# Kernel optimization log

Measured on AMD Instinct MI355X. Metric: run time of the kernel, lower is better.

The kernel has to match this reference:

```python
import jax, jax.numpy as jnp
import numpy as np
import math

B = 1024
G = 34  # grid_dim = 17*2
C = 4
SCENT = 19


def _scent_kernel_np():
    h = w = SCENT
    mx, my = 0.5 * h, 0.5 * w
    sx, sy = h / 4.0, w / 4.0
    x = np.linspace(0.0, h, h)
    y = np.linspace(0.0, w, w)
    X, Y = np.meshgrid(x, y, indexing='ij')
    z = (1.0 / (2.0 * math.pi * sx * sy)) * np.exp(-(((X - mx) ** 2) / (2 * sx ** 2) + ((Y - my) ** 2) / (2 * sy ** 2)))
    return (z * 80.0).astype(np.float32)


def setup_inputs() -> dict:
    key = jax.random.key(0)
    k1, k2, k3, k4 = jax.random.split(key, 4)
    cell = jax.random.uniform(k1, (B, C, G, G), dtype=jnp.float32)
    food = (jax.random.uniform(k2, (B, G, G), dtype=jnp.float32) > 0.97).astype(jnp.float32)
    fc1_w = jax.random.normal(k3, (64, 12), dtype=jnp.float32) * (1.0 / np.sqrt(12))
    fc1_b = jnp.zeros((64,), dtype=jnp.float32)
    fc2_w = jax.random.normal(k4, (4, 64), dtype=jnp.float32) * (1.0 / np.sqrt(64))
    fc2_b = jnp.zeros((4,), dtype=jnp.float32)
    scent_kernel = jnp.asarray(_scent_kernel_np())
    return {"cell": cell, "food": food, "fc1_w": fc1_w, "fc1_b": fc1_b,
            "fc2_w": fc2_w, "fc2_b": fc2_b, "scent_kernel": scent_kernel, "steps": 32}


def _conv(x, w, pad, groups):
    # x: [B, Cin, H, W], w: [Cout, Cin/groups, kh, kw]; cross-correlation like torch
    return jax.lax.conv_general_dilated(
        x, w, window_strides=(1, 1), padding=[(pad, pad), (pad, pad)],
        feature_group_count=groups, dimension_numbers=('NCHW', 'OIHW', 'NCHW'))


def _maxpool3(x):
    # 3x3 max pool, stride 1, pad 1 (pad value -inf, matching torch MaxPool2d semantics)
    return jax.lax.reduce_window(x, -jnp.inf, jax.lax.max, (1, 1, 3, 3), (1, 1, 1, 1),
                                 [(0, 0), (0, 0), (1, 1), (1, 1)])


def _forward(cell, food, fc1_w, fc1_b, fc2_w, fc2_b, scent_kernel, steps):
    dx = jnp.outer(jnp.array([1., 2., 1.], jnp.float32), jnp.array([-1., 0., 1.], jnp.float32)) / 8.0
    dy = dx.T
    kdx = jnp.tile(dx[None, None], (4, 1, 1, 1))  # depthwise, groups=4
    kdy = jnp.tile(dy[None, None], (4, 1, 1, 1))

    # perceive_scent: 19x19 gaussian conv, padding 9
    scent = _conv(food[:, None], scent_kernel[None, None], 9, 1)[:, 0]  # [B,G,G]

    def step(cell, _):
        cell = cell.at[:, 3].set(scent)
        # current living count per batch (cells in channel 0 above 0.8)
        cl = jnp.sum((cell[:, 0] > 0.8).astype(jnp.float32), axis=(1, 2))
        pre_mask = _maxpool3(cell[:, 0:1]) > 0.1  # [B,1,G,G]
        # perception: x, sobel-x, sobel-y -> 12 channels
        y1 = _conv(cell, kdx, 1, 4)
        y2 = _conv(cell, kdy, 1, 4)
        y = jnp.concatenate([cell, y1, y2], axis=1)  # [B,12,G,G]
        # tiny MLP per pixel (torch transposes dims 1<->3; linear over channels is equivalent)
        h = jax.nn.relu(jnp.einsum('bchw,oc->bohw', y, fc1_w) + fc1_b[None, :, None, None])
        upd = jnp.einsum('bchw,oc->bohw', h, fc2_w) + fc2_b[None, :, None, None]
        x = cell + upd
        post_mask = _maxpool3(x[:, 0:1]) > 0.1
        x = x * (pre_mask & post_mask).astype(x.dtype)
        x = jnp.clip(x, -10.0, 10.0)
        x = x.at[:, 0].set(jnp.clip(x[:, 0], 0.0, 1.0))
        # keep_k_largest: threshold = cl-th smallest (ascending sort index == cl); keep strictly greater
        flat = x[:, 0].reshape(B, -1)  # [B, G*G]
        srt = jnp.sort(flat, axis=1)
        kth = jnp.take_along_axis(srt, cl.astype(jnp.int32)[:, None], axis=1)  # [B,1] (gather clamps OOB)
        flat = jnp.where(flat > kth, flat, 0.0)
        x = x.at[:, 0].set(flat.reshape(B, G, G))
        return x, None

    cell, _ = jax.lax.scan(jax.checkpoint(step), cell, None, length=steps)
    total_pixel_val = cell[:, 0:1].sum(axis=(1, 2, 3))
    living_count = jnp.sum((cell[:, 0:1] > 0.1).astype(jnp.float32), axis=(1, 2, 3))
    return cell, food, total_pixel_val, living_count


def reference(cell, food, fc1_w, fc1_b, fc2_w, fc2_b, scent_kernel, steps):
    return _forward(cell, food, fc1_w, fc1_b, fc2_w, fc2_b, scent_kernel, steps)
```

## Files before the change

### kernel.cpp

```cpp
#include <hip/hip_runtime.h>
#include <stdint.h>

#define GD    34
#define GP    36
#define NPIX  1156
#define NT    256
#define NB    1024
#define TPR   7
#define TUSED 238

#define SCAN_PASS(KK) do {                                                         \
    if (wid == 0) {                                                                \
      const int base2 = lane << 4;                                                 \
      int c16[16]; int csum = 0;                                                   \
      _Pragma("unroll")                                                            \
      for (int j = 0; j < 16; ++j) { c16[j] = hist[base2+j]; hist[base2+j] = 0; csum += c16[j]; } \
      int inc = csum;                                                              \
      _Pragma("unroll")                                                            \
      for (int off2 = 1; off2 < 64; off2 <<= 1) { int vv = __shfl_up(inc, off2); if (lane >= off2) inc += vv; } \
      const int excl = inc - csum;                                                 \
      if ((KK) >= excl && (KK) < inc) {                                            \
        int rem = (KK) - excl; int cum = 0;                                        \
        _Pragma("unroll")                                                          \
        for (int j = 0; j < 16; ++j) {                                             \
          if (rem >= cum && rem < cum + c16[j]) { sel_bin = base2 + j; sel_rem = rem - cum; } \
          cum += c16[j];                                                           \
        }                                                                          \
      }                                                                            \
    }                                                                              \
  } while (0)

#define SCRN 4904

__global__ __launch_bounds__(NT) __attribute__((amdgpu_waves_per_eu(4, 4)))
void ca_kernel(const float* __restrict__ cell_in,
               const float* __restrict__ food_in,
               const float* __restrict__ fc1_w,
               const float* __restrict__ fc1_b,
               const float* __restrict__ fc2_w,
               const float* __restrict__ fc2_b,
               const float* __restrict__ sk_g,
               const int*   __restrict__ steps_p,
               float* __restrict__ out)
{
  __shared__ float cbuf[3][GP*GP];
  __shared__ float scratch[SCRN];
  __shared__ int   icl[2][4];
  __shared__ int   inzaz[4];
  __shared__ int   sel_bin, sel_rem;
  __shared__ float fsum[4];
  __shared__ int   lcnt[4];

  float* x0buf = scratch;
  float* x1s   = scratch + 1296;
  float* x2s   = scratch + 2452;
  int*   premi = (int*)(scratch + 3608);
  int*   hist  = (int*)(scratch + 1296);

  const int tid  = threadIdx.x;
  const int b    = blockIdx.x;
  const int lane = tid & 63;
  const int wid  = tid >> 6;
  const int nsteps = steps_p[0];

  const bool tval = (tid < TUSED);
  const int  trow = tval ? (tid / TPR) : 0;
  const int  c0   = tval ? ((tid % TPR) * 5) : 0;
  const int  nval = tval ? ((c0 <= 29) ? 5 : 4) : 0;
  const int  pb0  = tval ? ((trow+1)*GP + c0 + 1) : 37;
  const int  p0   = trow*GD + c0;

  for (int idx = tid; idx < 3*GP*GP; idx += NT) (&cbuf[0][0])[idx] = 0.f;
  for (int idx = tid; idx < SCRN;    idx += NT) scratch[idx] = 0.f;
  __syncthreads();

  float v3k[5];
  int cnt0 = 0;
#pragma unroll
  for (int j = 0; j < 5; ++j) {
    v3k[j] = 0.f;
    if (j < nval) {
      int p = p0 + j;
      const float* gi = cell_in + (size_t)b*4*NPIX + p;
      float v0 = gi[0], v1 = gi[NPIX], v2 = gi[2*NPIX], v3 = gi[3*NPIX];
      cbuf[0][pb0+j] = v0; cbuf[1][pb0+j] = v1; cbuf[2][pb0+j] = v2;
      v3k[j] = v3;
      cnt0 += (v0 > 0.8f) ? 1 : 0;
      scratch[(trow+9)*52 + (c0+j+9)] = food_in[(size_t)b*NPIX + p];
    }
  }
#pragma unroll
  for (int off = 32; off; off >>= 1) cnt0 += __shfl_down(cnt0, off);
  if (lane == 0) icl[0][wid] = cnt0;
  __syncthreads();

  float scent[5];
#pragma unroll
  for (int j = 0; j < 5; ++j) {
    float ssum = 0.f;
    if (j < nval) {
      for (int dr = 0; dr < 19; ++dr) {
        const float* frow = scratch + (trow+dr)*52 + (c0+j);
        const float* krow = sk_g + dr*19;
#pragma unroll
        for (int dc = 0; dc < 19; ++dc) ssum = fmaf(frow[dc], krow[dc], ssum);
      }
    }
    scent[j] = ssum;
  }
  __syncthreads();
  for (int idx = tid; idx < SCRN; idx += NT) scratch[idx] = 0.f;
  __syncthreads();
#pragma unroll
  for (int j = 0; j < 5; ++j) if (j < nval) x0buf[pb0+j] = scent[j];
  __syncthreads();
  float sxs[5], sys[5];
#pragma unroll
  for (int j = 0; j < 5; ++j) {
    const int bb = (j < nval) ? (pb0 + j) : pb0;
    float t00=x0buf[bb-GP-1], t01=x0buf[bb-GP], t02=x0buf[bb-GP+1];
    float t10=x0buf[bb-1],                      t12=x0buf[bb+1];
    float t20=x0buf[bb+GP-1], t21=x0buf[bb+GP], t22=x0buf[bb+GP+1];
    sxs[j] = ((t02 - t00) + 2.f*(t12 - t10) + (t22 - t20)) * 0.125f;
    sys[j] = ((t20 - t00) + 2.f*(t21 - t01) + (t22 - t02)) * 0.125f;
  }

  const float b2r0 = fc2_b[0], b2r1 = fc2_b[1], b2r2 = fc2_b[2], b2r3 = fc2_b[3];

  for (int s = 0; s < nsteps; ++s) {
    __syncthreads();
    float cm[7];
#pragma unroll
    for (int jc = 0; jc < 7; ++jc) {
      cm[jc] = 0.f;
      if (jc < nval + 2) {
        const int a = pb0 - 1 + jc;
        cm[jc] = fmaxf(fmaxf(cbuf[0][a-GP], cbuf[0][a]), cbuf[0][a+GP]);
      }
    }
    unsigned pm = 0;
#pragma unroll
    for (int j = 0; j < 5; ++j) {
      if (j < nval) {
        bool t = fmaxf(fmaxf(cm[j], cm[j+1]), cm[j+2]) > 0.1f;
        premi[pb0+j] = t ? 1 : 0;
        if (t) pm |= (1u << j);
      }
    }
    __syncthreads();
    int co[7];
#pragma unroll
    for (int jc = 0; jc < 7; ++jc) {
      co[jc] = 0;
      if (jc < nval + 2) {
        const int a = pb0 - 1 + jc;
        co[jc] = premi[a-GP] | premi[a] | premi[a+GP];
      }
    }
#pragma unroll
    for (int j = 0; j < 5; ++j) {
      int acti = (j < nval) ? (co[j] | co[j+1] | co[j+2]) : 0;
      if (__any(acti)) {
        const int bb = (j < nval) ? (pb0 + j) : pb0;
        float y0,y1,y2,y4,y5,y6,y8,y9,y10;
        {
          const float* cb = cbuf[0];
          float t00=cb[bb-GP-1], t01=cb[bb-GP], t02=cb[bb-GP+1];
          float t10=cb[bb-1],    t11=cb[bb],    t12=cb[bb+1];
          float t20=cb[bb+GP-1], t21=cb[bb+GP], t22=cb[bb+GP+1];
          y0 = t11;
          y4 = ((t02 - t00) + 2.f*(t12 - t10) + (t22 - t20)) * 0.125f;
          y8 = ((t20 - t00) + 2.f*(t21 - t01) + (t22 - t02)) * 0.125f;
        }
        {
          const float* cb = cbuf[1];
          float t00=cb[bb-GP-1], t01=cb[bb-GP], t02=cb[bb-GP+1];
          float t10=cb[bb-1],    t11=cb[bb],    t12=cb[bb+1];
          float t20=cb[bb+GP-1], t21=cb[bb+GP], t22=cb[bb+GP+1];
          y1 = t11;
          y5 = ((t02 - t00) + 2.f*(t12 - t10) + (t22 - t20)) * 0.125f;
          y9 = ((t20 - t00) + 2.f*(t21 - t01) + (t22 - t02)) * 0.125f;
        }
        {
          const float* cb = cbuf[2];
          float t00=cb[bb-GP-1], t01=cb[bb-GP], t02=cb[bb-GP+1];
          float t10=cb[bb-1],    t11=cb[bb],    t12=cb[bb+1];
          float t20=cb[bb+GP-1], t21=cb[bb+GP], t22=cb[bb+GP+1];
          y2 = t11;
          y6 = ((t02 - t00) + 2.f*(t12 - t10) + (t22 - t20)) * 0.125f;
          y10= ((t20 - t00) + 2.f*(t21 - t01) + (t22 - t02)) * 0.125f;
        }
        const float y3 = scent[j], y7 = sxs[j], y11 = sys[j];
        float u0 = b2r0, u1 = b2r1, u2 = b2r2, u3 = b2r3;
        for (int o = 0; o < 64; ++o) {
          const float* wr = fc1_w + o*12;
          float t = fc1_b[o];
          t = fmaf(y0, wr[0], t);  t = fmaf(y1, wr[1], t);
          t = fmaf(y2, wr[2], t);  t = fmaf(y3, wr[3], t);
          t = fmaf(y4, wr[4], t);  t = fmaf(y5, wr[5], t);
          t = fmaf(y6, wr[6], t);  t = fmaf(y7, wr[7], t);
          t = fmaf(y8, wr[8], t);  t = fmaf(y9, wr[9], t);
          t = fmaf(y10, wr[10], t); t = fmaf(y11, wr[11], t);
          t = fmaxf(t, 0.f);
          u0 = fmaf(t, fc2_w[o],     u0);
          u1 = fmaf(t, fc2_w[64+o],  u1);
          u2 = fmaf(t, fc2_w[128+o], u2);
          u3 = fmaf(t, fc2_w[192+o], u3);
        }
        v3k[j] = y3 + u3;
        if (j < nval) {
          x0buf[bb]    = y0 + u0;
          x1s[p0 + j]  = y1 + u1;
          x2s[p0 + j]  = y2 + u2;
        }
      }
    }
    __syncthreads();
    unsigned pq = 0;
    float midv[5];
#pragma unroll
    for (int j = 0; j < 5; ++j) midv[j] = 0.f;
    if (pm) {
      float dm[7];
#pragma unroll
      for (int jc = 0; jc < 7; ++jc) {
        dm[jc] = 0.f;
        if (jc < nval + 2) {
          const int a = pb0 - 1 + jc;
          float u = x0buf[a-GP], m = x0buf[a], d = x0buf[a+GP];
          dm[jc] = fmaxf(fmaxf(u, m), d);
          if (jc >= 1 && jc <= 5) midv[jc-1] = m;
        }
      }
#pragma unroll
      for (int j = 0; j < 5; ++j)
        if (fmaxf(fmaxf(dm[j], dm[j+1]), dm[j+2]) > 0.1f) pq |= (1u << j);
    }
    int packed = 0;
    float v0s[5];
#pragma unroll
    for (int j = 0; j < 5; ++j) {
      v0s[j] = 0.f;
      if (j < nval) {
        bool alive = ((pm >> j) & 1u) && ((pq >> j) & 1u);
        float v0 = 0.f, v1 = 0.f, v2 = 0.f, v3 = 0.f;
        if (alive) {
          v0 = fminf(fmaxf(midv[j],      0.f),  1.f);
          v1 = fminf(fmaxf(x1s[p0+j], -10.f), 10.f);
          v2 = fminf(fmaxf(x2s[p0+j], -10.f), 10.f);
          v3 = fminf(fmaxf(v3k[j],    -10.f), 10.f);
        }
        cbuf[1][pb0+j] = v1; cbuf[2][pb0+j] = v2; v3k[j] = v3;
        v0s[j] = v0;
        int zer = (v0 == 0.f) ? 1 : 0;
        int azf = (zer && v1 == 0.f && v2 == 0.f && v3 == 0.f) ? 1 : 0;
        packed += zer + (azf << 16);
      }
    }
#pragma unroll
    for (int off = 32; off; off >>= 1) packed += __shfl_down(packed, off);
    if (lane == 0) inzaz[wid] = packed;
    __syncthreads();
    const int t01 = inzaz[0]+inzaz[1]+inzaz[2]+inzaz[3];
    const int nz = t01 & 0xffff, az = t01 >> 16;
    const int cl = icl[s&1][0]+icl[s&1][1]+icl[s&1][2]+icl[s&1][3];
    const int k  = (cl < NPIX) ? cl : (NPIX-1);
    float kth = 0.f;
    if (k >= nz) {
      hist[tid] = 0; hist[tid+256] = 0; hist[tid+512] = 0; hist[tid+768] = 0;
      __syncthreads();
      const int k2 = k - nz;
#pragma unroll
      for (int j = 0; j < 5; ++j) {
        unsigned u = __float_as_uint(v0s[j]);
        if (j < nval && u != 0u) atomicAdd(&hist[u >> 20], 1);
      }
      __syncthreads();
      SCAN_PASS(k2);
      __syncthreads();
      const int bin1 = sel_bin; const int kr2 = sel_rem;
#pragma unroll
      for (int j = 0; j < 5; ++j) {
        unsigned u = __float_as_uint(v0s[j]);
        if (j < nval && u != 0u && (u >> 20) == (unsigned)bin1)
          atomicAdd(&hist[(u >> 10) & 1023u], 1);
      }
      __syncthreads();
      SCAN_PASS(kr2);
      __syncthreads();
      const int bin2 = sel_bin; const int kr3 = sel_rem;
      const unsigned pref2 = (((unsigned)bin1) << 10) | (unsigned)bin2;
#pragma unroll
      for (int j = 0; j < 5; ++j) {
        unsigned u = __float_as_uint(v0s[j]);
        if (j < nval && u != 0u && (u >> 10) == pref2)
          atomicAdd(&hist[u & 1023u], 1);
      }
      __syncthreads();
      SCAN_PASS(kr3);
      __syncthreads();
      kth = __uint_as_float((((unsigned)bin1) << 20) | (((unsigned)bin2) << 10) | (unsigned)sel_bin);
    }
    int cnt = 0;
#pragma unroll
    for (int j = 0; j < 5; ++j) {
      if (j < nval) {
        float w0 = (v0s[j] > kth) ? v0s[j] : 0.f;
        cbuf[0][pb0+j] = w0;
        cnt += (w0 > 0.8f) ? 1 : 0;
      }
    }
#pragma unroll
    for (int off = 32; off; off >>= 1) cnt += __shfl_down(cnt, off);
    if (lane == 0) icl[(s+1)&1][wid] = cnt;
    if (az == NPIX) break;
  }

  const size_t CELL_N = (size_t)4*NPIX*NB;
  const size_t FOOD_N = (size_t)NPIX*NB;
  float tp = 0.f; int lcv = 0;
#pragma unroll
  for (int j = 0; j < 5; ++j) {
    if (j < nval) {
      const int p = p0 + j;
      float c0v = cbuf[0][pb0+j], c1 = cbuf[1][pb0+j], c2 = cbuf[2][pb0+j];
      size_t go = (size_t)b*4*NPIX + p;
      out[go]          = c0v;
      out[go +   NPIX] = c1;
      out[go + 2*NPIX] = c2;
      out[go + 3*NPIX] = v3k[j];
      out[CELL_N + (size_t)b*NPIX + p] = food_in[(size_t)b*NPIX + p];
      tp += c0v;
      lcv += (c0v > 0.1f) ? 1 : 0;
    }
  }
#pragma unroll
  for (int off = 32; off; off >>= 1) { tp += __shfl_down(tp, off); lcv += __shfl_down(lcv, off); }
  if (lane == 0) { fsum[wid] = tp; lcnt[wid] = lcv; }
  __syncthreads();
  if (tid == 0) {
    out[CELL_N + FOOD_N + b]      = fsum[0]+fsum[1]+fsum[2]+fsum[3];
    out[CELL_N + FOOD_N + NB + b] = (float)(lcnt[0]+lcnt[1]+lcnt[2]+lcnt[3]);
  }
}

extern "C" void kernel_launch(void* const* d_in, const int* in_sizes, int n_in,
                              void* d_out, int out_size, void* d_ws, size_t ws_size,
                              hipStream_t stream) {
  const float* cell  = (const float*)d_in[0];
  const float* food  = (const float*)d_in[1];
  const float* fc1w  = (const float*)d_in[2];
  const float* fc1b  = (const float*)d_in[3];
  const float* fc2w  = (const float*)d_in[4];
  const float* fc2b  = (const float*)d_in[5];
  const float* sk    = (const float*)d_in[6];
  const int*   steps = (const int*)d_in[7];
  float* out = (float*)d_out;
  ca_kernel<<<NB, NT, 0, stream>>>(cell, food, fc1w, fc1b, fc2w, fc2b, sk, steps, out);
}
```

Before: 265.3 us.

## Double threads per block, compute 5x5 activity mask directly, pack MLP weights

Doubles the block to 512 threads, each handling 3 pixels instead of 5, so more parallelism per cell grid. The pre-mask/activity check now uses a 5x5 max directly from the cell buffer, which removes the premi shared array and one barrier per step. A small pre-kernel packs fc1/fc2 weights into one interleaved row per hidden unit, so each hidden unit reads contiguous weights. Trade-offs are register pressure under the 8 waves/EU limit and an extra kernel launch. The scent stage is still computed with 19x19 loops per pixel, now shared across more threads.

Result: no change. 270.0 us (+1.8%).

```diff
diff --git a/kernel.cpp b/kernel.cpp
--- a/kernel.cpp
+++ b/kernel.cpp
@@ -4,10 +4,12 @@
 #define GD    34
 #define GP    36
 #define NPIX  1156
-#define NT    256
+#define NT    512
+#define NW    8
 #define NB    1024
-#define TPR   7
-#define TUSED 238
+#define TPR   12
+#define TUSED 408
+#define SP    3
 
 #define SCAN_PASS(KK) do {                                                         \
     if (wid == 0) {                                                                \
@@ -30,31 +32,42 @@
     }                                                                              \
   } while (0)
 
-#define SCRN 4904
-
-__global__ __launch_bounds__(NT) __attribute__((amdgpu_waves_per_eu(4, 4)))
+#define SCRN 3608
+
+__global__ void pack_w(const float* __restrict__ fc1_w, const float* __restrict__ fc1_b,
+                       const float* __restrict__ fc2_w, float* __restrict__ wp) {
+  int o = threadIdx.x;
+  if (o < 64) {
+#pragma unroll
+    for (int j = 0; j < 12; ++j) wp[o*20+j] = fc1_w[o*12+j];
+    wp[o*20+12] = fc1_b[o];
+    wp[o*20+13] = fc2_w[o];
+    wp[o*20+14] = fc2_w[64+o];
+    wp[o*20+15] = fc2_w[128+o];
+    wp[o*20+16] = fc2_w[192+o];
+  }
+}
+
+__global__ __launch_bounds__(NT) __attribute__((amdgpu_waves_per_eu(8, 8)))
 void ca_kernel(const float* __restrict__ cell_in,
                const float* __restrict__ food_in,
-               const float* __restrict__ fc1_w,
-               const float* __restrict__ fc1_b,
-               const float* __restrict__ fc2_w,
                const float* __restrict__ fc2_b,
                const float* __restrict__ sk_g,
                const int*   __restrict__ steps_p,
+               const float* __restrict__ wp,
                float* __restrict__ out)
 {
   __shared__ float cbuf[3][GP*GP];
   __shared__ float scratch[SCRN];
-  __shared__ int   icl[2][4];
-  __shared__ int   inzaz[4];
+  __shared__ int   icl[2][NW];
+  __shared__ int   inzaz[NW];
   __shared__ int   sel_bin, sel_rem;
-  __shared__ float fsum[4];
-  __shared__ int   lcnt[4];
+  __shared__ float fsum[NW];
+  __shared__ int   lcnt[NW];
 
   float* x0buf = scratch;
   float* x1s   = scratch + 1296;
   float* x2s   = scratch + 2452;
-  int*   premi = (int*)(scratch + 3608);
   int*   hist  = (int*)(scratch + 1296);
 
   const int tid  = threadIdx.x;
@@ -65,19 +78,24 @@
 
   const bool tval = (tid < TUSED);
   const int  trow = tval ? (tid / TPR) : 0;
-  const int  c0   = tval ? ((tid % TPR) * 5) : 0;
-  const int  nval = tval ? ((c0 <= 29) ? 5 : 4) : 0;
+  const int  c0   = tval ? ((tid % TPR) * SP) : 0;
+  const int  nval = tval ? ((c0 <= 31) ? 3 : 1) : 0;
   const int  pb0  = tval ? ((trow+1)*GP + c0 + 1) : 37;
   const int  p0   = trow*GD + c0;
 
+  const int r0b = pb0 - (c0 + 1);
+  const int rm1 = r0b - GP, rp1 = r0b + GP;
+  const int rm2 = (r0b - 2*GP < 0) ? 0 : (r0b - 2*GP);
+  const int rp2 = (r0b + 2*GP > 35*GP) ? 35*GP : (r0b + 2*GP);
+
   for (int idx = tid; idx < 3*GP*GP; idx += NT) (&cbuf[0][0])[idx] = 0.f;
   for (int idx = tid; idx < SCRN;    idx += NT) scratch[idx] = 0.f;
   __syncthreads();
 
-  float v3k[5];
+  float v3k[SP];
   int cnt0 = 0;
 #pragma unroll
-  for (int j = 0; j < 5; ++j) {
+  for (int j = 0; j < SP; ++j) {
     v3k[j] = 0.f;
     if (j < nval) {
       int p = p0 + j;
@@ -94,9 +112,9 @@
   if (lane == 0) icl[0][wid] = cnt0;
   __syncthreads();
 
-  float scent[5];
-#pragma unroll
-  for (int j = 0; j < 5; ++j) {
+  float scent[SP];
+#pragma unroll
+  for (int j = 0; j < SP; ++j) {
     float ssum = 0.f;
     if (j < nval) {
       for (int dr = 0; dr < 19; ++dr) {
@@ -112,11 +130,11 @@
   for (int idx = tid; idx < SCRN; idx += NT) scratch[idx] = 0.f;
   __syncthreads();
 #pragma unroll
-  for (int j = 0; j < 5; ++j) if (j < nval) x0buf[pb0+j] = scent[j];
-  __syncthreads();
-  float sxs[5], sys[5];
-#pragma unroll
-  for (int j = 0; j < 5; ++j) {
+  for (int j = 0; j < SP; ++j) if (j < nval) x0buf[pb0+j] = scent[j];
+  __syncthreads();
+  float sxs[SP], sys[SP];
+#pragma unroll
+  for (int j = 0; j < SP; ++j) {
     const int bb = (j < nval) ? (pb0 + j) : pb0;
     float t00=x0buf[bb-GP-1], t01=x0buf[bb-GP], t02=x0buf[bb-GP+1];
     float t10=x0buf[bb-1],                      t12=x0buf[bb+1];
@@ -129,37 +147,27 @@
 
   for (int s = 0; s < nsteps; ++s) {
     __syncthreads();
-    float cm[7];
+    float cm3[7], cm5[7];
 #pragma unroll
     for (int jc = 0; jc < 7; ++jc) {
-      cm[jc] = 0.f;
-      if (jc < nval + 2) {
-        const int a = pb0 - 1 + jc;
-        cm[jc] = fmaxf(fmaxf(cbuf[0][a-GP], cbuf[0][a]), cbuf[0][a+GP]);
+      cm3[jc] = 0.f; cm5[jc] = 0.f;
+      if (jc < nval + 4) {
+        int pc = c0 - 1 + jc;
+        pc = (pc < 0) ? 0 : ((pc > 35) ? 35 : pc);
+        const float* cb = cbuf[0];
+        float c3 = fmaxf(fmaxf(cb[rm1+pc], cb[r0b+pc]), cb[rp1+pc]);
+        cm3[jc] = c3;
+        cm5[jc] = fmaxf(fmaxf(cb[rm2+pc], cb[rp2+pc]), c3);
       }
     }
     unsigned pm = 0;
 #pragma unroll
-    for (int j = 0; j < 5; ++j) {
-      if (j < nval) {
-        bool t = fmaxf(fmaxf(cm[j], cm[j+1]), cm[j+2]) > 0.1f;
-        premi[pb0+j] = t ? 1 : 0;
-        if (t) pm |= (1u << j);
-      }
-    }
-    __syncthreads();
-    int co[7];
-#pragma unroll
-    for (int jc = 0; jc < 7; ++jc) {
-      co[jc] = 0;
-      if (jc < nval + 2) {
-        const int a = pb0 - 1 + jc;
-        co[jc] = premi[a-GP] | premi[a] | premi[a+GP];
-      }
-    }
-#pragma unroll
-    for (int j = 0; j < 5; ++j) {
-      int acti = (j < nval) ? (co[j] | co[j+1] | co[j+2]) : 0;
+    for (int j = 0; j < SP; ++j)
+      if (j < nval && fmaxf(fmaxf(cm3[j+1], cm3[j+2]), cm3[j+3]) > 0.1f) pm |= (1u << j);
+#pragma unroll
+    for (int j = 0; j < SP; ++j) {
+      float a5 = fmaxf(fmaxf(fmaxf(cm5[j], cm5[j+1]), fmaxf(cm5[j+2], cm5[j+3])), cm5[j+4]);
+      int acti = (j < nval) && (a5 > 0.1f);
       if (__any(acti)) {
         const int bb = (j < nval) ? (pb0 + j) : pb0;
         float y0,y1,y2,y4,y5,y6,y8,y9,y10;
@@ -193,8 +201,8 @@
         const float y3 = scent[j], y7 = sxs[j], y11 = sys[j];
         float u0 = b2r0, u1 = b2r1, u2 = b2r2, u3 = b2r3;
         for (int o = 0; o < 64; ++o) {
-          const float* wr = fc1_w + o*12;
-          float t = fc1_b[o];
+          const float* wr = wp + o*20;
+          float t = wr[12];
           t = fmaf(y0, wr[0], t);  t = fmaf(y1, wr[1], t);
           t = fmaf(y2, wr[2], t);  t = fmaf(y3, wr[3], t);
           t = fmaf(y4, wr[4], t);  t = fmaf(y5, wr[5], t);
@@ -202,44 +210,44 @@
           t = fmaf(y8, wr[8], t);  t = fmaf(y9, wr[9], t);
           t = fmaf(y10, wr[10], t); t = fmaf(y11, wr[11], t);
           t = fmaxf(t, 0.f);
-          u0 = fmaf(t, fc2_w[o],     u0);
-          u1 = fmaf(t, fc2_w[64+o],  u1);
-          u2 = fmaf(t, fc2_w[128+o], u2);
-          u3 = fmaf(t, fc2_w[192+o], u3);
+          u0 = fmaf(t, wr[13], u0);
+          u1 = fmaf(t, wr[14], u1);
+          u2 = fmaf(t, wr[15], u2);
+          u3 = fmaf(t, wr[16], u3);
         }
         v3k[j] = y3 + u3;
         if (j < nval) {
-          x0buf[bb]    = y0 + u0;
-          x1s[p0 + j]  = y1 + u1;
-          x2s[p0 + j]  = y2 + u2;
+          x0buf[bb]   = y0 + u0;
+          x1s[p0 + j] = y1 + u1;
+          x2s[p0 + j] = y2 + u2;
         }
       }
     }
     __syncthreads();
     unsigned pq = 0;
-    float midv[5];
-#pragma unroll
-    for (int j = 0; j < 5; ++j) midv[j] = 0.f;
+    float midv[SP];
+#pragma unroll
+    for (int j = 0; j < SP; ++j) midv[j] = 0.f;
     if (pm) {
-      float dm[7];
-#pragma unroll
-      for (int jc = 0; jc < 7; ++jc) {
+      float dm[SP+2];
+#pragma unroll
+      for (int jc = 0; jc < SP+2; ++jc) {
         dm[jc] = 0.f;
         if (jc < nval + 2) {
           const int a = pb0 - 1 + jc;
           float u = x0buf[a-GP], m = x0buf[a], d = x0buf[a+GP];
           dm[jc] = fmaxf(fmaxf(u, m), d);
-          if (jc >= 1 && jc <= 5) midv[jc-1] = m;
-        }
-      }
-#pragma unroll
-      for (int j = 0; j < 5; ++j)
+          if (jc >= 1 && jc <= nval) midv[jc-1] = m;
+        }
+      }
+#pragma unroll
+      for (int j = 0; j < SP; ++j)
         if (fmaxf(fmaxf(dm[j], dm[j+1]), dm[j+2]) > 0.1f) pq |= (1u << j);
     }
     int packed = 0;
-    float v0s[5];
-#pragma unroll
-    for (int j = 0; j < 5; ++j) {
+    float v0s[SP];
+#pragma unroll
+    for (int j = 0; j < SP; ++j) {
       v0s[j] = 0.f;
       if (j < nval) {
         bool alive = ((pm >> j) & 1u) && ((pq >> j) & 1u);
@@ -261,17 +269,18 @@
     for (int off = 32; off; off >>= 1) packed += __shfl_down(packed, off);
     if (lane == 0) inzaz[wid] = packed;
     __syncthreads();
-    const int t01 = inzaz[0]+inzaz[1]+inzaz[2]+inzaz[3];
+    int t01 = 0, cl = 0;
+#pragma unroll
+    for (int w = 0; w < NW; ++w) { t01 += inzaz[w]; cl += icl[s&1][w]; }
     const int nz = t01 & 0xffff, az = t01 >> 16;
-    const int cl = icl[s&1][0]+icl[s&1][1]+icl[s&1][2]+icl[s&1][3];
     const int k  = (cl < NPIX) ? cl : (NPIX-1);
     float kth = 0.f;
     if (k >= nz) {
-      hist[tid] = 0; hist[tid+256] = 0; hist[tid+512] = 0; hist[tid+768] = 0;
+      hist[tid] = 0; hist[tid+512] = 0;
       __syncthreads();
       const int k2 = k - nz;
 #pragma unroll
-      for (int j = 0; j < 5; ++j) {
+      for (int j = 0; j < SP; ++j) {
         unsigned u = __float_as_uint(v0s[j]);
         if (j < nval && u != 0u) atomicAdd(&hist[u >> 20], 1);
       }
@@ -280,7 +289,7 @@
       __syncthreads();
       const int bin1 = sel_bin; const int kr2 = sel_rem;
 #pragma unroll
-      for (int j = 0; j < 5; ++j) {
+      for (int j = 0; j < SP; ++j) {
         unsigned u = __float_as_uint(v0s[j]);
         if (j < nval && u != 0u && (u >> 20) == (unsigned)bin1)
           atomicAdd(&hist[(u >> 10) & 1023u], 1);
@@ -291,7 +300,7 @@
       const int bin2 = sel_bin; const int kr3 = sel_rem;
       const unsigned pref2 = (((unsigned)bin1) << 10) | (unsigned)bin2;
 #pragma unroll
-      for (int j = 0; j < 5; ++j) {
+      for (int j = 0; j < SP; ++j) {
         unsigned u = __float_as_uint(v0s[j]);
         if (j < nval && u != 0u && (u >> 10) == pref2)
           atomicAdd(&hist[u & 1023u], 1);
@@ -303,7 +312,7 @@
     }
     int cnt = 0;
 #pragma unroll
-    for (int j = 0; j < 5; ++j) {
+    for (int j = 0; j < SP; ++j) {
       if (j < nval) {
         float w0 = (v0s[j] > kth) ? v0s[j] : 0.f;
         cbuf[0][pb0+j] = w0;
@@ -320,7 +329,7 @@
   const size_t FOOD_N = (size_t)NPIX*NB;
   float tp = 0.f; int lcv = 0;
 #pragma unroll
-  for (int j = 0; j < 5; ++j) {
+  for (int j = 0; j < SP; ++j) {
     if (j < nval) {
       const int p = p0 + j;
       float c0v = cbuf[0][pb0+j], c1 = cbuf[1][pb0+j], c2 = cbuf[2][pb0+j];
@@ -339,8 +348,11 @@
   if (lane == 0) { fsum[wid] = tp; lcnt[wid] = lcv; }
   __syncthreads();
   if (tid == 0) {
-    out[CELL_N + FOOD_N + b]      = fsum[0]+fsum[1]+fsum[2]+fsum[3];
-    out[CELL_N + FOOD_N + NB + b] = (float)(lcnt[0]+lcnt[1]+lcnt[2]+lcnt[3]);
+    float tps = 0.f; int lcs = 0;
+#pragma unroll
+    for (int w = 0; w < NW; ++w) { tps += fsum[w]; lcs += lcnt[w]; }
+    out[CELL_N + FOOD_N + b]      = tps;
+    out[CELL_N + FOOD_N + NB + b] = (float)lcs;
   }
 }
 
@@ -356,5 +368,7 @@
   const float* sk    = (const float*)d_in[6];
   const int*   steps = (const int*)d_in[7];
   float* out = (float*)d_out;
-  ca_kernel<<<NB, NT, 0, stream>>>(cell, food, fc1w, fc1b, fc2w, fc2b, sk, steps, out);
+  float* wp  = (float*)d_ws;
+  pack_w<<<1, 64, 0, stream>>>(fc1w, fc1b, fc2w, wp);
+  ca_kernel<<<NB, NT, 0, stream>>>(cell, food, fc2b, sk, steps, wp, out);
 }
```
